# Kernel optimization log

Measured on AMD Instinct MI355X. Metric: run time of the kernel, lower is better.

## Reference

```python
import jax, jax.numpy as jnp
import numpy as np

NUM_ITERS = 5
TEMP = 0.1


def setup_inputs() -> dict:
    key = jax.random.key(0)
    k1, k2 = jax.random.split(key)
    pred_masks = jax.random.uniform(k1, (1, 100, 512, 512), dtype=jnp.float32)
    gt_masks = jax.random.uniform(k2, (50, 512, 512), dtype=jnp.float32)
    return {"pred_masks": pred_masks, "gt_masks": gt_masks}


def reference(pred_masks, gt_masks):
    # pred_masks: [B=1, K, H, W]; gt_masks: [N, H, W]
    gt = gt_masks[None]  # [1, N, H, W]
    # cost[b,k,n] = 1 - <pred_k, gt_n> over HW
    cost = 1.0 - jnp.einsum('bkhw,bnhw->bkn', pred_masks, gt)
    log_alpha = -cost / TEMP  # [1, K, N]
    for _ in range(NUM_ITERS):
        log_alpha = log_alpha - jax.nn.logsumexp(log_alpha, axis=2, keepdims=True)
        log_alpha = log_alpha - jax.nn.logsumexp(log_alpha, axis=1, keepdims=True)
    return jnp.exp(log_alpha)
```

## Files before the change

kernel.cpp:

```cpp
#include <hip/hip_runtime.h>
#include <math.h>

#define HW       262144
#define TOTSTEPS (HW / 32)
#define MROWS    100
#define NCOLS    50
#define OUTSZ    (MROWS * NCOLS)

typedef __attribute__((ext_vector_type(8))) _Float16 f16x8;
typedef __attribute__((ext_vector_type(2))) __fp16   fp16x2;
typedef __attribute__((ext_vector_type(4))) float    f32x4;

#define ABYTES   14400
#define BUFBYTES 24576

typedef __attribute__((address_space(1))) const unsigned int GU32;
typedef __attribute__((address_space(3))) unsigned int LU32;

__device__ __forceinline__ void split_f16(const float4& v0, const float4& v1,
                                          f16x8& hi, f16x8& lo) {
  float xs[8] = {v0.x, v0.y, v0.z, v0.w, v1.x, v1.y, v1.z, v1.w};
  union { fp16x2 p[4]; f16x8 v; } H, L;
#pragma unroll
  for (int j = 0; j < 4; ++j) {
    H.p[j] = __builtin_amdgcn_cvt_pkrtz(xs[2 * j], xs[2 * j + 1]);
    float l0 = xs[2 * j]     - (float)H.p[j][0];
    float l1 = xs[2 * j + 1] - (float)H.p[j][1];
    L.p[j] = __builtin_amdgcn_cvt_pkrtz(l0, l1);
  }
  hi = H.v; lo = L.v;
}

__global__ __launch_bounds__(256, 2) void dm_phase1(
    const float* __restrict__ pred, const float* __restrict__ gt,
    float* __restrict__ partial, int nblk) {
  __shared__ unsigned char smem[3 * BUFBYTES];

  const int b    = blockIdx.x;
  const int tid  = threadIdx.x;
  const int lane = tid & 63;
  const int wid  = tid >> 6;
  const int wi = wid >> 1, wj = wid & 1;
  const int g = lane >> 4, r = lane & 15;

  const int k0s = (int)(((long)b * TOTSTEPS) / nblk);
  const int k1s = (int)(((long)(b + 1) * TOTSTEPS) / nblk);
  const int nst = k1s - k0s;

  const float* srcb[6];
#pragma unroll
  for (int it = 0; it < 6; ++it) {
    int s = it * 256 + tid;
    const float* p;
    if (s < 900) {
      int row = s / 9;
      int off = (s - row * 9) * 16;
      if (off > 112) off = 112;
      p = pred + (size_t)row * HW + (off >> 2);
    } else if (s < 1350) {
      int s2 = s - 900;
      int row = s2 / 9;
      int off = (s2 - row * 9) * 16;
      if (off > 112) off = 112;
      p = gt + (size_t)row * HW + (off >> 2);
    } else {
      p = pred + ((s - 1350) & 7) * 4;
    }
    srcb[it] = p;
  }

  auto STAGE = [&](unsigned char* bufb, int kf) {
#pragma unroll
    for (int it = 0; it < 6; ++it)
      __builtin_amdgcn_global_load_lds((GU32*)(srcb[it] + kf),
          (LU32*)(bufb + (it * 256 + wid * 64) * 16), 16, 0, 0);
  };

  f32x4 acc[4][2] = {};

  auto COMPUTE = [&](const unsigned char* bufb) {
    f16x8 bh[2], bl[2];
#pragma unroll
    for (int nf = 0; nf < 2; ++nf) {
      int R = wj * 32 + nf * 16 + r;
      if (R > NCOLS - 1) R = NCOLS - 1;
      const unsigned char* rowb = bufb + ABYTES + R * 144;
      float4 v0 = *(const float4*)(rowb + 32 * g);
      float4 v1 = *(const float4*)(rowb + 32 * g + 16);
      split_f16(v0, v1, bh[nf], bl[nf]);
    }
#pragma unroll
    for (int mf = 0; mf < 4; ++mf) {
      if (wi == 0 || mf < 3) {
        int R = wi * 64 + mf * 16 + r;
        if (R > MROWS - 1) R = MROWS - 1;
        const unsigned char* rowb = bufb + R * 144;
        float4 v0 = *(const float4*)(rowb + 32 * g);
        float4 v1 = *(const float4*)(rowb + 32 * g + 16);
        f16x8 ah, al;
        split_f16(v0, v1, ah, al);
#pragma unroll
        for (int nf = 0; nf < 2; ++nf) {
          acc[mf][nf] = __builtin_amdgcn_mfma_f32_16x16x32_f16(ah, bh[nf], acc[mf][nf], 0, 0, 0);
          acc[mf][nf] = __builtin_amdgcn_mfma_f32_16x16x32_f16(al, bh[nf], acc[mf][nf], 0, 0, 0);
          acc[mf][nf] = __builtin_amdgcn_mfma_f32_16x16x32_f16(ah, bl[nf], acc[mf][nf], 0, 0, 0);
        }
      }
    }
  };

  STAGE(smem, k0s << 5);
  if (nst > 1) STAGE(smem + BUFBYTES, (k0s + 1) << 5);

  int qc = 0;
  for (int s = 0; s < nst; ++s) {
    if (s + 1 < nst) asm volatile("s_waitcnt vmcnt(6)" ::: "memory");
    else             asm volatile("s_waitcnt vmcnt(0)" ::: "memory");
    __builtin_amdgcn_s_barrier();
    COMPUTE(smem + qc * BUFBYTES);
    if (s + 2 < nst) {
      int qs = qc + 2; if (qs >= 3) qs -= 3;
      STAGE(smem + qs * BUFBYTES, (k0s + s + 2) << 5);
    }
    qc = (qc == 2) ? 0 : qc + 1;
  }

#pragma unroll
  for (int mf = 0; mf < 4; ++mf) {
#pragma unroll
    for (int nf = 0; nf < 2; ++nf) {
#pragma unroll
      for (int qq = 0; qq < 4; ++qq) {
        int row = wi * 64 + mf * 16 + g * 4 + qq;
        int col = wj * 32 + nf * 16 + r;
        if (row < MROWS && col < NCOLS)
          partial[(size_t)b * OUTSZ + row * NCOLS + col] = acc[mf][nf][qq];
      }
    }
  }
}

template <int NB>
__global__ void dm_reduce(const float* __restrict__ partial,
                          double* __restrict__ la0) {
  const int tid = threadIdx.x, wid = tid >> 6, lane = tid & 63;
  const int pbase = blockIdx.x * 16 + wid * 4;
  if (pbase >= OUTSZ) return;
  constexpr int IT = NB / 64;
  float4 v[IT];
#pragma unroll
  for (int i = 0; i < IT; ++i)
    v[i] = *(const float4*)(partial + (size_t)(lane + 64 * i) * OUTSZ + pbase);
  double d0 = 0, d1 = 0, d2 = 0, d3 = 0;
#pragma unroll
  for (int i = 0; i < IT; ++i) {
    d0 += (double)v[i].x; d1 += (double)v[i].y;
    d2 += (double)v[i].z; d3 += (double)v[i].w;
  }
#pragma unroll
  for (int off = 32; off; off >>= 1) {
    d0 += __shfl_xor(d0, off);
    d1 += __shfl_xor(d1, off);
    d2 += __shfl_xor(d2, off);
    d3 += __shfl_xor(d3, off);
  }
  if (lane == 0) {
    la0[pbase + 0] = (d0 - 1.0) * 10.0;
    la0[pbase + 1] = (d1 - 1.0) * 10.0;
    la0[pbase + 2] = (d2 - 1.0) * 10.0;
    la0[pbase + 3] = (d3 - 1.0) * 10.0;
  }
}

__global__ __launch_bounds__(256) void dm_sinkhorn(const double* __restrict__ la_in,
                                                   float* __restrict__ out) {
  __shared__ double la[OUTSZ];
  __shared__ double rp[MROWS];
  __shared__ double cp[NCOLS];
  const int t = threadIdx.x;
  for (int p = t; p < OUTSZ; p += 256) la[p] = la_in[p];
  if (t < NCOLS) cp[t] = 0.0;
  __syncthreads();
  for (int it = 0; it < 5; ++it) {
    if (t < 2 * MROWS) {
      int row = t >> 1, sl = t & 1;
      double m = -1e300;
      for (int j = sl; j < NCOLS; j += 2) m = fmax(m, la[row * NCOLS + j] - cp[j]);
      float s = 0.f;
      for (int j = sl; j < NCOLS; j += 2)
        s += __expf((float)(la[row * NCOLS + j] - cp[j] - m));
      double mo = __shfl_xor(m, 1); float so = __shfl_xor(s, 1);
      double mn = fmax(m, mo);
      s = s * __expf((float)(m - mn)) + so * __expf((float)(mo - mn));
      if (sl == 0) rp[row] = mn + (double)__logf(s);
    }
    __syncthreads();
    if (t < 4 * NCOLS) {
      int col = t >> 2, sl = t & 3;
      double m = -1e300;
      for (int i = sl; i < MROWS; i += 4) m = fmax(m, la[i * NCOLS + col] - rp[i]);
      float s = 0.f;
      for (int i = sl; i < MROWS; i += 4)
        s += __expf((float)(la[i * NCOLS + col] - rp[i] - m));
#pragma unroll
      for (int off = 1; off < 4; off <<= 1) {
        double mo = __shfl_xor(m, off); float so = __shfl_xor(s, off);
        double mn = fmax(m, mo);
        s = s * __expf((float)(m - mn)) + so * __expf((float)(mo - mn));
        m = mn;
      }
      if (sl == 0) cp[col] = m + (double)__logf(s);
    }
    __syncthreads();
  }
  for (int p = t; p < OUTSZ; p += 256)
    out[p] = __expf((float)(la[p] - rp[p / NCOLS] - cp[p % NCOLS]));
}

extern "C" void kernel_launch(void* const* d_in, const int* in_sizes, int n_in,
                              void* d_out, int out_size, void* d_ws, size_t ws_size,
                              hipStream_t stream) {
  const float* pred = (const float*)d_in[0];
  const float* gt   = (const float*)d_in[1];
  float* out = (float*)d_out;

  auto fits = [&](int nb) {
    return ((size_t)nb * OUTSZ * sizeof(float) + OUTSZ * sizeof(double)) <= ws_size;
  };
  int nblk = fits(512) ? 512 : 256;

  float*  partial = (float*)d_ws;
  double* la0 = (double*)((char*)d_ws + (size_t)nblk * OUTSZ * sizeof(float));

  dm_phase1<<<nblk, 256, 0, stream>>>(pred, gt, partial, nblk);
  if (nblk == 512) dm_reduce<512><<<(OUTSZ + 15) / 16, 256, 0, stream>>>(partial, la0);
  else             dm_reduce<256><<<(OUTSZ + 15) / 16, 256, 0, stream>>>(partial, la0);
  dm_sinkhorn<<<1, 256, 0, stream>>>(la0, out);
}
```

Baseline: 75.68 us.

## Replace direct global-to-LDS loads with register-staged double buffering, raise occupancy and block count

Swaps the triple-buffered global_load_lds pipeline for loads into registers followed by explicit LDS writes into two ping-pong buffers, with a barrier after each compute. Cutting LDS use to two buffers allows three blocks per CU, and the grid grows to 768 blocks so the partial reduction is spread over more work. This trades the asynchronous direct-to-LDS path for extra VGPR pressure and a full __syncthreads per step, and the reduce kernel must now read more partial sums.

```diff
diff --git a/kernel.cpp b/kernel.cpp
--- a/kernel.cpp
+++ b/kernel.cpp
@@ -14,9 +14,6 @@
 #define ABYTES   14400
 #define BUFBYTES 24576
 
-typedef __attribute__((address_space(1))) const unsigned int GU32;
-typedef __attribute__((address_space(3))) unsigned int LU32;
-
 __device__ __forceinline__ void split_f16(const float4& v0, const float4& v1,
                                           f16x8& hi, f16x8& lo) {
   float xs[8] = {v0.x, v0.y, v0.z, v0.w, v1.x, v1.y, v1.z, v1.w};
@@ -31,10 +28,10 @@
   hi = H.v; lo = L.v;
 }
 
-__global__ __launch_bounds__(256, 2) void dm_phase1(
+__global__ __launch_bounds__(256, 3) void dm_phase1(
     const float* __restrict__ pred, const float* __restrict__ gt,
     float* __restrict__ partial, int nblk) {
-  __shared__ unsigned char smem[3 * BUFBYTES];
+  __shared__ unsigned char smem[2 * BUFBYTES];
 
   const int b    = blockIdx.x;
   const int tid  = threadIdx.x;
@@ -47,33 +44,34 @@
   const int k1s = (int)(((long)(b + 1) * TOTSTEPS) / nblk);
   const int nst = k1s - k0s;
 
-  const float* srcb[6];
+  const float* srcp[6];
+  int   ldso[6];
+  bool  ok[6];
 #pragma unroll
   for (int it = 0; it < 6; ++it) {
     int s = it * 256 + tid;
-    const float* p;
-    if (s < 900) {
-      int row = s / 9;
-      int off = (s - row * 9) * 16;
-      if (off > 112) off = 112;
-      p = pred + (size_t)row * HW + (off >> 2);
-    } else if (s < 1350) {
-      int s2 = s - 900;
-      int row = s2 / 9;
-      int off = (s2 - row * 9) * 16;
-      if (off > 112) off = 112;
-      p = gt + (size_t)row * HW + (off >> 2);
-    } else {
-      p = pred + ((s - 1350) & 7) * 4;
-    }
-    srcb[it] = p;
-  }
-
-  auto STAGE = [&](unsigned char* bufb, int kf) {
+    ok[it] = s < 1350;
+    int row, off;
+    const float* base;
+    int lbase;
+    if (s < 900)      { row = s / 9;         off = (s - row * 9) * 16;       base = pred; lbase = 0; }
+    else              { int s2 = s - 900;
+                        row = s2 / 9;        off = (s2 - row * 9) * 16;      base = gt;   lbase = ABYTES;
+                        if (s >= 1350) { row = 0; off = 0; } }
+    int soff = off > 112 ? 112 : off;
+    srcp[it] = base + (size_t)row * HW + (soff >> 2);
+    ldso[it] = lbase + row * 144 + soff;
+  }
+
+  auto LOADREG = [&](float4 (&rg)[6], int kf) {
 #pragma unroll
     for (int it = 0; it < 6; ++it)
-      __builtin_amdgcn_global_load_lds((GU32*)(srcb[it] + kf),
-          (LU32*)(bufb + (it * 256 + wid * 64) * 16), 16, 0, 0);
+      if (ok[it]) rg[it] = *(const float4*)(srcp[it] + kf);
+  };
+  auto WRITE = [&](unsigned char* bufb, float4 (&rg)[6]) {
+#pragma unroll
+    for (int it = 0; it < 6; ++it)
+      if (ok[it]) *(float4*)(bufb + ldso[it]) = rg[it];
   };
 
   f32x4 acc[4][2] = {};
@@ -109,20 +107,29 @@
     }
   };
 
-  STAGE(smem, k0s << 5);
-  if (nst > 1) STAGE(smem + BUFBYTES, (k0s + 1) << 5);
-
-  int qc = 0;
-  for (int s = 0; s < nst; ++s) {
-    if (s + 1 < nst) asm volatile("s_waitcnt vmcnt(6)" ::: "memory");
-    else             asm volatile("s_waitcnt vmcnt(0)" ::: "memory");
-    __builtin_amdgcn_s_barrier();
-    COMPUTE(smem + qc * BUFBYTES);
+  unsigned char* buf0 = smem;
+  unsigned char* buf1 = smem + BUFBYTES;
+
+  float4 ra[6], rb[6];
+  LOADREG(ra, k0s << 5);
+  WRITE(buf0, ra);
+  if (nst > 1) LOADREG(rb, (k0s + 1) << 5);
+  __syncthreads();
+
+  for (int s = 0; s < nst; s += 2) {
+    if (s + 1 < nst) {
+      WRITE(buf1, rb);
+      if (s + 2 < nst) LOADREG(ra, (k0s + s + 2) << 5);
+    }
+    COMPUTE(buf0);
+    __syncthreads();
+    if (s + 1 >= nst) break;
     if (s + 2 < nst) {
-      int qs = qc + 2; if (qs >= 3) qs -= 3;
-      STAGE(smem + qs * BUFBYTES, (k0s + s + 2) << 5);
-    }
-    qc = (qc == 2) ? 0 : qc + 1;
+      WRITE(buf0, ra);
+      if (s + 3 < nst) LOADREG(rb, (k0s + s + 3) << 5);
+    }
+    COMPUTE(buf1);
+    __syncthreads();
   }
 
 #pragma unroll
@@ -227,13 +234,14 @@
   auto fits = [&](int nb) {
     return ((size_t)nb * OUTSZ * sizeof(float) + OUTSZ * sizeof(double)) <= ws_size;
   };
-  int nblk = fits(512) ? 512 : 256;
+  int nblk = fits(768) ? 768 : (fits(512) ? 512 : 256);
 
   float*  partial = (float*)d_ws;
   double* la0 = (double*)((char*)d_ws + (size_t)nblk * OUTSZ * sizeof(float));
 
   dm_phase1<<<nblk, 256, 0, stream>>>(pred, gt, partial, nblk);
-  if (nblk == 512) dm_reduce<512><<<(OUTSZ + 15) / 16, 256, 0, stream>>>(partial, la0);
-  else             dm_reduce<256><<<(OUTSZ + 15) / 16, 256, 0, stream>>>(partial, la0);
+  if (nblk == 768)      dm_reduce<768><<<(OUTSZ + 15) / 16, 256, 0, stream>>>(partial, la0);
+  else if (nblk == 512) dm_reduce<512><<<(OUTSZ + 15) / 16, 256, 0, stream>>>(partial, la0);
+  else                  dm_reduce<256><<<(OUTSZ + 15) / 16, 256, 0, stream>>>(partial, la0);
   dm_sinkhorn<<<1, 256, 0, stream>>>(la0, out);
 }
```

New measurement: 124.1 us. 64.0% more time.

## Stage wider K chunks with double buffering and fixed 256 blocks

Applied to the files above, without the earlier changes.

Phase 1 now stages 128-float K chunks per row (four times wider) into two 80KB LDS buffers, double-buffered, instead of 32-float chunks in a triple buffer. The grid is fixed at 256 blocks with 8 stages each, and the adaptive choice of 512 blocks is dropped. The aim is to cut per-stage barrier and waitcnt overhead and issue larger, more contiguous global loads. In exchange, occupancy falls to one block per CU because of the large LDS footprint, and more barriers are added per stage pair.

```diff
diff --git a/kernel.cpp b/kernel.cpp
--- a/kernel.cpp
+++ b/kernel.cpp
@@ -2,17 +2,19 @@
 #include <math.h>
 
 #define HW       262144
-#define TOTSTEPS (HW / 32)
 #define MROWS    100
 #define NCOLS    50
 #define OUTSZ    (MROWS * NCOLS)
+#define NBLK     256
+#define NST      8
 
 typedef __attribute__((ext_vector_type(8))) _Float16 f16x8;
 typedef __attribute__((ext_vector_type(2))) __fp16   fp16x2;
 typedef __attribute__((ext_vector_type(4))) float    f32x4;
 
-#define ABYTES   14400
-#define BUFBYTES 24576
+#define ROWB     528
+#define ABROWS   150
+#define BUFBYTES 81920
 
 typedef __attribute__((address_space(1))) const unsigned int GU32;
 typedef __attribute__((address_space(3))) unsigned int LU32;
@@ -31,10 +33,10 @@
   hi = H.v; lo = L.v;
 }
 
-__global__ __launch_bounds__(256, 2) void dm_phase1(
+__global__ __launch_bounds__(256, 1) void dm_phase1(
     const float* __restrict__ pred, const float* __restrict__ gt,
-    float* __restrict__ partial, int nblk) {
-  __shared__ unsigned char smem[3 * BUFBYTES];
+    float* __restrict__ partial) {
+  __shared__ unsigned char smem[2 * BUFBYTES];
 
   const int b    = blockIdx.x;
   const int tid  = threadIdx.x;
@@ -43,86 +45,81 @@
   const int wi = wid >> 1, wj = wid & 1;
   const int g = lane >> 4, r = lane & 15;
 
-  const int k0s = (int)(((long)b * TOTSTEPS) / nblk);
-  const int k1s = (int)(((long)(b + 1) * TOTSTEPS) / nblk);
-  const int nst = k1s - k0s;
-
-  const float* srcb[6];
-#pragma unroll
-  for (int it = 0; it < 6; ++it) {
+  const int kbase = b << 10;
+
+  const float* srcp[20];
+#pragma unroll
+  for (int it = 0; it < 20; ++it) {
     int s = it * 256 + tid;
-    const float* p;
-    if (s < 900) {
-      int row = s / 9;
-      int off = (s - row * 9) * 16;
-      if (off > 112) off = 112;
-      p = pred + (size_t)row * HW + (off >> 2);
-    } else if (s < 1350) {
-      int s2 = s - 900;
-      int row = s2 / 9;
-      int off = (s2 - row * 9) * 16;
-      if (off > 112) off = 112;
-      p = gt + (size_t)row * HW + (off >> 2);
-    } else {
-      p = pred + ((s - 1350) & 7) * 4;
-    }
-    srcb[it] = p;
-  }
-
-  auto STAGE = [&](unsigned char* bufb, int kf) {
-#pragma unroll
-    for (int it = 0; it < 6; ++it)
-      __builtin_amdgcn_global_load_lds((GU32*)(srcb[it] + kf),
+    int row = s / 33;
+    int c   = s - row * 33;
+    if (c > 31) c = 31;
+    if (row >= ABROWS) { row = ABROWS - 1; c = 31; }
+    const float* base = row < MROWS ? pred + (size_t)row * HW
+                                    : gt + (size_t)(row - MROWS) * HW;
+    srcp[it] = base + kbase + c * 4;
+  }
+
+  auto STAGE = [&](unsigned char* bufb, int s) {
+#pragma unroll
+    for (int it = 0; it < 20; ++it)
+      __builtin_amdgcn_global_load_lds((GU32*)(srcp[it] + (s << 7)),
           (LU32*)(bufb + (it * 256 + wid * 64) * 16), 16, 0, 0);
   };
 
   f32x4 acc[4][2] = {};
 
   auto COMPUTE = [&](const unsigned char* bufb) {
-    f16x8 bh[2], bl[2];
-#pragma unroll
-    for (int nf = 0; nf < 2; ++nf) {
-      int R = wj * 32 + nf * 16 + r;
-      if (R > NCOLS - 1) R = NCOLS - 1;
-      const unsigned char* rowb = bufb + ABYTES + R * 144;
-      float4 v0 = *(const float4*)(rowb + 32 * g);
-      float4 v1 = *(const float4*)(rowb + 32 * g + 16);
-      split_f16(v0, v1, bh[nf], bl[nf]);
-    }
-#pragma unroll
-    for (int mf = 0; mf < 4; ++mf) {
-      if (wi == 0 || mf < 3) {
-        int R = wi * 64 + mf * 16 + r;
-        if (R > MROWS - 1) R = MROWS - 1;
-        const unsigned char* rowb = bufb + R * 144;
+#pragma unroll
+    for (int kk = 0; kk < 4; ++kk) {
+      f16x8 bh[2], bl[2];
+#pragma unroll
+      for (int nf = 0; nf < 2; ++nf) {
+        int R = wj * 32 + nf * 16 + r;
+        if (R > NCOLS - 1) R = NCOLS - 1;
+        const unsigned char* rowb = bufb + (MROWS + R) * ROWB + kk * 128;
         float4 v0 = *(const float4*)(rowb + 32 * g);
         float4 v1 = *(const float4*)(rowb + 32 * g + 16);
-        f16x8 ah, al;
-        split_f16(v0, v1, ah, al);
-#pragma unroll
-        for (int nf = 0; nf < 2; ++nf) {
-          acc[mf][nf] = __builtin_amdgcn_mfma_f32_16x16x32_f16(ah, bh[nf], acc[mf][nf], 0, 0, 0);
-          acc[mf][nf] = __builtin_amdgcn_mfma_f32_16x16x32_f16(al, bh[nf], acc[mf][nf], 0, 0, 0);
-          acc[mf][nf] = __builtin_amdgcn_mfma_f32_16x16x32_f16(ah, bl[nf], acc[mf][nf], 0, 0, 0);
+        split_f16(v0, v1, bh[nf], bl[nf]);
+      }
+#pragma unroll
+      for (int mf = 0; mf < 4; ++mf) {
+        if (wi == 0 || mf < 3) {
+          int R = wi * 64 + mf * 16 + r;
+          if (R > MROWS - 1) R = MROWS - 1;
+          const unsigned char* rowb = bufb + R * ROWB + kk * 128;
+          float4 v0 = *(const float4*)(rowb + 32 * g);
+          float4 v1 = *(const float4*)(rowb + 32 * g + 16);
+          f16x8 ah, al;
+          split_f16(v0, v1, ah, al);
+#pragma unroll
+          for (int nf = 0; nf < 2; ++nf) {
+            acc[mf][nf] = __builtin_amdgcn_mfma_f32_16x16x32_f16(ah, bh[nf], acc[mf][nf], 0, 0, 0);
+            acc[mf][nf] = __builtin_amdgcn_mfma_f32_16x16x32_f16(al, bh[nf], acc[mf][nf], 0, 0, 0);
+            acc[mf][nf] = __builtin_amdgcn_mfma_f32_16x16x32_f16(ah, bl[nf], acc[mf][nf], 0, 0, 0);
+          }
         }
       }
     }
   };
 
-  STAGE(smem, k0s << 5);
-  if (nst > 1) STAGE(smem + BUFBYTES, (k0s + 1) << 5);
-
-  int qc = 0;
-  for (int s = 0; s < nst; ++s) {
-    if (s + 1 < nst) asm volatile("s_waitcnt vmcnt(6)" ::: "memory");
+  unsigned char* buf0 = smem;
+  unsigned char* buf1 = smem + BUFBYTES;
+
+  STAGE(buf0, 0);
+  STAGE(buf1, 1);
+  for (int s = 0; s < NST; s += 2) {
+    asm volatile("s_waitcnt vmcnt(20)" ::: "memory");
+    __builtin_amdgcn_s_barrier();
+    COMPUTE(buf0);
+    __builtin_amdgcn_s_barrier();
+    if (s + 2 < NST) STAGE(buf0, s + 2);
+    if (s + 2 < NST) asm volatile("s_waitcnt vmcnt(20)" ::: "memory");
     else             asm volatile("s_waitcnt vmcnt(0)" ::: "memory");
     __builtin_amdgcn_s_barrier();
-    COMPUTE(smem + qc * BUFBYTES);
-    if (s + 2 < nst) {
-      int qs = qc + 2; if (qs >= 3) qs -= 3;
-      STAGE(smem + qs * BUFBYTES, (k0s + s + 2) << 5);
-    }
-    qc = (qc == 2) ? 0 : qc + 1;
+    COMPUTE(buf1);
+    __builtin_amdgcn_s_barrier();
+    if (s + 3 < NST) STAGE(buf1, s + 3);
   }
 
 #pragma unroll
@@ -224,16 +221,10 @@
   const float* gt   = (const float*)d_in[1];
   float* out = (float*)d_out;
 
-  auto fits = [&](int nb) {
-    return ((size_t)nb * OUTSZ * sizeof(float) + OUTSZ * sizeof(double)) <= ws_size;
-  };
-  int nblk = fits(512) ? 512 : 256;
-
   float*  partial = (float*)d_ws;
-  double* la0 = (double*)((char*)d_ws + (size_t)nblk * OUTSZ * sizeof(float));
-
-  dm_phase1<<<nblk, 256, 0, stream>>>(pred, gt, partial, nblk);
-  if (nblk == 512) dm_reduce<512><<<(OUTSZ + 15) / 16, 256, 0, stream>>>(partial, la0);
-  else             dm_reduce<256><<<(OUTSZ + 15) / 16, 256, 0, stream>>>(partial, la0);
+  double* la0 = (double*)((char*)d_ws + (size_t)NBLK * OUTSZ * sizeof(float));
+
+  dm_phase1<<<NBLK, 256, 0, stream>>>(pred, gt, partial);
+  dm_reduce<NBLK><<<(OUTSZ + 15) / 16, 256, 0, stream>>>(partial, la0);
   dm_sinkhorn<<<1, 256, 0, stream>>>(la0, out);
 }
```

Measured after the change: 84.68 us. 11.9% more time.
